# Optimization experiments

Hardware: AMD Instinct MI355X
Metric: run time of the kernel (lower is better)

## Reference

```python
import jax, jax.numpy as jnp
import numpy as np
import math

D_MODEL, NHEAD, D_FF = 1024, 16, 4096
S_TGT, S_MEM, BATCH = 2048, 2048, 2
D_K = D_MODEL // NHEAD
EPS = 1e-5


def _linear_params(key, d_in, d_out):
    kw, kb = jax.random.split(key)
    w = jax.random.normal(kw, (d_in, d_out), jnp.float32) * 0.02
    b = jax.random.normal(kb, (d_out,), jnp.float32) * 0.02
    return w, b


def setup_inputs() -> dict:
    key = jax.random.key(0)
    ks = jax.random.split(key, 16)
    inp = {
        "tgt": jax.random.normal(ks[0], (S_TGT, BATCH, D_MODEL), jnp.float32),
        "memory": jax.random.normal(ks[1], (S_MEM, BATCH, D_MODEL), jnp.float32),
    }
    # self-attn params
    inp["sa_wq"], inp["sa_bq"] = _linear_params(ks[2], D_MODEL, D_MODEL)
    inp["sa_wk"], inp["sa_bk"] = _linear_params(ks[3], D_MODEL, D_MODEL)
    inp["sa_wv"], inp["sa_bv"] = _linear_params(ks[4], D_MODEL, D_MODEL)
    inp["sa_wo"], inp["sa_bo"] = _linear_params(ks[5], D_MODEL, D_MODEL)
    # cross-attn params
    inp["ca_wq"], inp["ca_bq"] = _linear_params(ks[6], D_MODEL, D_MODEL)
    inp["ca_wk"], inp["ca_bk"] = _linear_params(ks[7], D_MODEL, D_MODEL)
    inp["ca_wv"], inp["ca_bv"] = _linear_params(ks[8], D_MODEL, D_MODEL)
    inp["ca_wo"], inp["ca_bo"] = _linear_params(ks[9], D_MODEL, D_MODEL)
    # FFN params
    inp["ff_w1"], inp["ff_b1"] = _linear_params(ks[10], D_MODEL, D_FF)
    inp["ff_w2"], inp["ff_b2"] = _linear_params(ks[11], D_FF, D_MODEL)
    # LayerNorm params
    for i, k in zip((1, 2, 3), (ks[12], ks[13], ks[14])):
        inp[f"ln{i}_g"] = jnp.ones((D_MODEL,), jnp.float32)
        inp[f"ln{i}_b"] = jnp.zeros((D_MODEL,), jnp.float32)
    # masks: causal for self-attn, full for cross-attn (1 = keep, 0 = masked)
    inp["tgt_mask"] = jnp.tril(jnp.ones((S_TGT, S_TGT), jnp.int32))
    inp["memory_mask"] = jnp.ones((S_TGT, S_MEM), jnp.int32)
    return inp


def layer_norm(x, g, b):
    mu = jnp.mean(x, axis=-1, keepdims=True)
    var = jnp.mean(jnp.square(x - mu), axis=-1, keepdims=True)
    return (x - mu) * jax.lax.rsqrt(var + EPS) * g + b


def mha(xq, xkv, wq, bq, wk, bk, wv, bv, wo, bo, mask):
    # xq: [Sq,B,D], xkv: [Sk,B,D], mask: [Sq,Sk] (1 keep / 0 masked)
    Sq, B, _ = xq.shape
    Sk = xkv.shape[0]
    q = (xq @ wq + bq).reshape(Sq, B, NHEAD, D_K)
    k = (xkv @ wk + bk).reshape(Sk, B, NHEAD, D_K)
    v = (xkv @ wv + bv).reshape(Sk, B, NHEAD, D_K)
    scores = jnp.einsum("qbhd,kbhd->bhqk", q, k) / math.sqrt(D_K)
    scores = jnp.where(mask[None, None, :, :] == 0, -1e9, scores)
    attn = jax.nn.softmax(scores, axis=-1)
    ctx = jnp.einsum("bhqk,kbhd->bqhd", attn, v).reshape(B, Sq, D_MODEL)
    out = ctx @ wo + bo  # [B,Sq,D]
    return out.transpose(1, 0, 2)  # [Sq,B,D]


def reference(tgt, memory,
              sa_wq, sa_bq, sa_wk, sa_bk, sa_wv, sa_bv, sa_wo, sa_bo,
              ca_wq, ca_bq, ca_wk, ca_bk, ca_wv, ca_bv, ca_wo, ca_bo,
              ff_w1, ff_b1, ff_w2, ff_b2,
              ln1_g, ln1_b, ln2_g, ln2_b, ln3_g, ln3_b,
              tgt_mask, memory_mask):
    # dropout is identity (eval mode)
    x = tgt + mha(tgt, tgt, sa_wq, sa_bq, sa_wk, sa_bk, sa_wv, sa_bv,
                  sa_wo, sa_bo, tgt_mask)
    x = layer_norm(x, ln1_g, ln1_b)
    x = x + mha(x, memory, ca_wq, ca_bq, ca_wk, ca_bk, ca_wv, ca_bv,
                ca_wo, ca_bo, memory_mask)
    x = layer_norm(x, ln2_g, ln2_b)
    ffn = jax.nn.relu(x @ ff_w1 + ff_b1) @ ff_w2 + ff_b2
    x = layer_norm(x + ffn, ln3_g, ln3_b)
    return x
```

## Files before the change

### kernel.cpp

```cpp
#include <hip/hip_runtime.h>
#include <cstdint>
#include <cstddef>


typedef __bf16 bf16;
typedef __attribute__((ext_vector_type(4))) float f32x4;
typedef __attribute__((ext_vector_type(8))) __bf16 bf16x8;
typedef __attribute__((ext_vector_type(4))) __bf16 bf16x4;
typedef __attribute__((ext_vector_type(2))) __bf16 bf16x2;

#define MFMA(a, b, c) __builtin_amdgcn_mfma_f32_16x16x32_bf16((a), (b), (c), 0, 0, 0)

constexpr int D_MODEL = 1024;
constexpr int S_LEN   = 2048;
constexpr int BATCH   = 2;
constexpr int M_ROWS  = S_LEN * BATCH;

struct bfp { bf16 h, l; };
__device__ __forceinline__ bfp fsplit(float f) {
  bfp r;
  r.h = (bf16)f;
  r.l = (bf16)(f - (float)r.h);
  return r;
}

typedef const void __attribute__((address_space(1))) gas_void;
typedef void __attribute__((address_space(3))) las_void;
__device__ __forceinline__ void glds16(const void* g, void* l) {
  __builtin_amdgcn_global_load_lds((gas_void*)g, (las_void*)l, 16, 0, 0);
}

__global__ void wcast_t(const float* __restrict__ W, bf16* __restrict__ Th,
                        int K, int N) {
  __shared__ float t[32][33];
  const int kt = blockIdx.x * 32, nt = blockIdx.y * 32;
  const int tx = threadIdx.x, ty = threadIdx.y;
#pragma unroll
  for (int i = 0; i < 4; ++i)
    t[ty * 4 + i][tx] = W[(size_t)(kt + ty * 4 + i) * N + nt + tx];
  __syncthreads();
#pragma unroll
  for (int i = 0; i < 4; ++i) {
    int n = nt + ty * 4 + i;
    Th[(size_t)n * K + kt + tx] = (bf16)t[tx][ty * 4 + i];
  }
}

__global__ void act_split(const float* __restrict__ X, bf16* __restrict__ H,
                          bf16* __restrict__ L) {
  const size_t i = ((size_t)blockIdx.x * 256 + threadIdx.x) * 4;
  float4 v = *reinterpret_cast<const float4*>(&X[i]);
  bf16x4 h, l;
  bfp s0 = fsplit(v.x); h[0] = s0.h; l[0] = s0.l;
  bfp s1 = fsplit(v.y); h[1] = s1.h; l[1] = s1.l;
  bfp s2 = fsplit(v.z); h[2] = s2.h; l[2] = s2.l;
  bfp s3 = fsplit(v.w); h[3] = s3.h; l[3] = s3.l;
  *reinterpret_cast<bf16x4*>(&H[i]) = h;
  *reinterpret_cast<bf16x4*>(&L[i]) = l;
}

__launch_bounds__(256)
__global__ void gemm_split(const bf16* __restrict__ Ah_g, const bf16* __restrict__ Al_g,
                           const bf16* __restrict__ Bh_g,
                           const float* __restrict__ bias,
                           float* Cf, bf16* Ch, bf16* Cl,
                           int N, int K, int ldb, int flags) {
  __shared__ bf16 sAh[4096], sAl[4096], sBh[4096];
  const int tid = threadIdx.x, ln = tid & 63, w = tid >> 6;
  const int g = ln >> 4, lr = ln & 15;
  const int wr = w >> 1, wc = w & 1;
  const int m0 = blockIdx.y * 128, n0 = blockIdx.x * 128;
  const int kz = K / gridDim.z;
  const int kbeg = blockIdx.z * kz, kend = kbeg + kz;

  f32x4 acc[4][4] = {};

  for (int k0 = kbeg; k0 < kend; k0 += 32) {
    __syncthreads();
#pragma unroll
    for (int i = 0; i < 2; ++i) {
      const int r = w * 32 + i * 16 + (ln >> 2);
      const int co = (ln & 3) * 8;
      const int lb = (w * 32 + i * 16) * 32;
      glds16(Ah_g + (size_t)(m0 + r) * K + k0 + co, &sAh[lb]);
      glds16(Al_g + (size_t)(m0 + r) * K + k0 + co, &sAl[lb]);
      glds16(Bh_g + (size_t)(n0 + r) * ldb + k0 + co, &sBh[lb]);
    }
    __syncthreads();

    bf16x8 ah[4], al[4], bh[4];
#pragma unroll
    for (int mi = 0; mi < 4; ++mi) {
      const int r = wr * 64 + mi * 16 + lr;
      ah[mi] = *reinterpret_cast<const bf16x8*>(&sAh[r * 32 + g * 8]);
      al[mi] = *reinterpret_cast<const bf16x8*>(&sAl[r * 32 + g * 8]);
    }
#pragma unroll
    for (int ni = 0; ni < 4; ++ni) {
      const int r = wc * 64 + ni * 16 + lr;
      bh[ni] = *reinterpret_cast<const bf16x8*>(&sBh[r * 32 + g * 8]);
    }
#pragma unroll
    for (int mi = 0; mi < 4; ++mi)
#pragma unroll
      for (int ni = 0; ni < 4; ++ni) {
        acc[mi][ni] = MFMA(ah[mi], bh[ni], acc[mi][ni]);
        acc[mi][ni] = MFMA(al[mi], bh[ni], acc[mi][ni]);
      }
  }

  const size_t MN = (size_t)M_ROWS * N;
#pragma unroll
  for (int mi = 0; mi < 4; ++mi)
#pragma unroll
    for (int ni = 0; ni < 4; ++ni) {
      const int col = n0 + wc * 64 + ni * 16 + lr;
      const float bv = ((flags & 16) && blockIdx.z == 0) ? bias[col] : 0.f;
#pragma unroll
      for (int r = 0; r < 4; ++r) {
        const int row = m0 + wr * 64 + mi * 16 + g * 4 + r;
        float v = acc[mi][ni][r] + bv;
        if (flags & 1) v = fmaxf(v, 0.f);
        const size_t off = (size_t)row * N + col;
        if (flags & 32) {
          Cf[blockIdx.z * MN + off] = v;
        } else if (flags & 2) {
          atomicAdd(&Cf[off], v);
        } else if (flags & 4) {
          Ch[off] = (bf16)v;
        } else if (flags & 8) {
          bfp sp = fsplit(v);
          Ch[off] = sp.h;
          Cl[off] = sp.l;
        } else {
          Cf[off] = v;
        }
      }
    }
}

__launch_bounds__(256)
__global__ void attn_kernel(const bf16* __restrict__ Qg, const bf16* __restrict__ Kg,
                            const bf16* __restrict__ Vg, int qs, int kvs,
                            bf16* __restrict__ Ch, bf16* __restrict__ Cl, int causal) {
  __shared__ bf16 Kl[2][64 * 64];
  __shared__ bf16 Vt[2][64][72];
  __shared__ bf16 Pl[4][32][68];
  const int tid = threadIdx.x, ln = tid & 63, w = tid >> 6;
  const int g = ln >> 4, lr = ln & 15;
  const int qt = blockIdx.x, bh = blockIdx.y;
  const int b = bh >> 4, h = bh & 15;
  const int q0 = qt * 128 + w * 32;

  const int krow8 = ln >> 3, d8 = ln & 7;
  const int dq = tid >> 4, kp = tid & 15;

  bf16x8 aq[2][2];
#pragma unroll
  for (int mf = 0; mf < 2; ++mf)
#pragma unroll
    for (int kk = 0; kk < 2; ++kk)
      aq[mf][kk] = *reinterpret_cast<const bf16x8*>(
          &Qg[((size_t)(q0 + mf * 16 + lr) * BATCH + b) * qs + h * 64 + kk * 32 + g * 8]);

  f32x4 acco[2][4] = {};
  float mrun[2][4], lrun[2][4];
#pragma unroll
  for (int mf = 0; mf < 2; ++mf)
#pragma unroll
    for (int r = 0; r < 4; ++r) { mrun[mf][r] = -1e30f; lrun[mf][r] = 0.f; }

  const int nkv = causal ? (qt * 2 + 2) : (S_LEN / 64);

  bf16x4 vreg[2][2];
  auto stageK = [&](int kv0, bf16* dst) {
#pragma unroll
    for (int i = 0; i < 2; ++i) {
      const int rbase = i * 32 + w * 8;
      const int row = rbase + krow8;
      glds16(Kg + (size_t)((kv0 + row) * BATCH + b) * kvs + h * 64 + ((d8 ^ (row & 7)) << 3),
             dst + rbase * 64);
    }
  };
  auto loadV = [&](int kv0) {
#pragma unroll
    for (int p = 0; p < 2; ++p) {
      const int k0v = p * 32 + kp * 2;
      vreg[p][0] = *reinterpret_cast<const bf16x4*>(
          &Vg[(size_t)((kv0 + k0v) * BATCH + b) * kvs + h * 64 + dq * 4]);
      vreg[p][1] = *reinterpret_cast<const bf16x4*>(
          &Vg[(size_t)((kv0 + k0v + 1) * BATCH + b) * kvs + h * 64 + dq * 4]);
    }
  };
  auto writeV = [&](int buf) {
#pragma unroll
    for (int p = 0; p < 2; ++p) {
      const int k0v = p * 32 + kp * 2;
#pragma unroll
      for (int i = 0; i < 4; ++i) {
        bf16x2 t2;
        t2[0] = vreg[p][0][i];
        t2[1] = vreg[p][1][i];
        *reinterpret_cast<bf16x2*>(&Vt[buf][dq * 4 + i][k0v]) = t2;
      }
    }
  };

  stageK(0, Kl[0]);
  loadV(0);
  writeV(0);
  __syncthreads();

  for (int kv = 0; kv < nkv; ++kv) {
    const int cur = kv & 1;
    const bool pre = (kv + 1 < nkv);
    if (pre) {
      stageK((kv + 1) * 64, Kl[cur ^ 1]);
      loadV((kv + 1) * 64);
    }
    const int kv0 = kv * 64;

    if (!(causal && kv0 > q0 + 31)) {
      const char* kbase = (const char*)Kl[cur];
      f32x4 s[2][4];
      __builtin_amdgcn_s_setprio(1);
#pragma unroll
      for (int mf = 0; mf < 2; ++mf)
#pragma unroll
        for (int c = 0; c < 4; ++c) {
          f32x4 a = {};
#pragma unroll
          for (int kk = 0; kk < 2; ++kk) {
            bf16x8 bk = *reinterpret_cast<const bf16x8*>(
                kbase + (c * 16 + lr) * 128 + ((((kk << 2) + g) ^ (lr & 7)) << 4));
            a = MFMA(aq[mf][kk], bk, a);
          }
          s[mf][c] = a;
        }
      __builtin_amdgcn_s_setprio(0);
#pragma unroll
      for (int mf = 0; mf < 2; ++mf)
#pragma unroll
        for (int c = 0; c < 4; ++c)
#pragma unroll
          for (int r = 0; r < 4; ++r) s[mf][c][r] *= 0.125f;

      if (causal && kv0 + 63 > q0) {
#pragma unroll
        for (int mf = 0; mf < 2; ++mf)
#pragma unroll
          for (int c = 0; c < 4; ++c) {
            const int key = kv0 + c * 16 + lr;
#pragma unroll
            for (int r = 0; r < 4; ++r)
              if (key > q0 + mf * 16 + g * 4 + r) s[mf][c][r] = -1e30f;
          }
      }

#pragma unroll
      for (int mf = 0; mf < 2; ++mf)
#pragma unroll
        for (int r = 0; r < 4; ++r) {
          float mx = fmaxf(fmaxf(s[mf][0][r], s[mf][1][r]), fmaxf(s[mf][2][r], s[mf][3][r]));
#pragma unroll
          for (int off = 8; off >= 1; off >>= 1) mx = fmaxf(mx, __shfl_xor(mx, off));
          const float mnew = fmaxf(mrun[mf][r], mx);
          const float sf = __expf(mrun[mf][r] - mnew);
          float pv[4], ps = 0.f;
#pragma unroll
          for (int c = 0; c < 4; ++c) { pv[c] = __expf(s[mf][c][r] - mnew); ps += pv[c]; }
          lrun[mf][r] = lrun[mf][r] * sf + ps;
          mrun[mf][r] = mnew;
#pragma unroll
          for (int t = 0; t < 4; ++t) acco[mf][t][r] *= sf;
#pragma unroll
          for (int c = 0; c < 4; ++c) Pl[w][mf * 16 + g * 4 + r][c * 16 + lr] = (bf16)pv[c];
        }

      __builtin_amdgcn_s_setprio(1);
#pragma unroll
      for (int mf = 0; mf < 2; ++mf) {
        bf16x8 ap0 = *reinterpret_cast<const bf16x8*>(&Pl[w][mf * 16 + lr][g * 8]);
        bf16x8 ap1 = *reinterpret_cast<const bf16x8*>(&Pl[w][mf * 16 + lr][32 + g * 8]);
#pragma unroll
        for (int t = 0; t < 4; ++t) {
          bf16x8 v0 = *reinterpret_cast<const bf16x8*>(&Vt[cur][t * 16 + lr][g * 8]);
          bf16x8 v1 = *reinterpret_cast<const bf16x8*>(&Vt[cur][t * 16 + lr][32 + g * 8]);
          acco[mf][t] = MFMA(ap0, v0, acco[mf][t]);
          acco[mf][t] = MFMA(ap1, v1, acco[mf][t]);
        }
      }
      __builtin_amdgcn_s_setprio(0);
    }

    if (pre) writeV(cur ^ 1);
    __syncthreads();
  }

#pragma unroll
  for (int mf = 0; mf < 2; ++mf)
#pragma unroll
    for (int r = 0; r < 4; ++r) {
      float l = lrun[mf][r];
#pragma unroll
      for (int off = 8; off >= 1; off >>= 1) l += __shfl_xor(l, off);
      lrun[mf][r] = 1.f / l;
    }
#pragma unroll
  for (int mf = 0; mf < 2; ++mf)
#pragma unroll
    for (int t = 0; t < 4; ++t)
#pragma unroll
      for (int r = 0; r < 4; ++r) {
        const int srow = q0 + mf * 16 + g * 4 + r;
        const size_t off = (size_t)(srow * BATCH + b) * D_MODEL + h * 64 + t * 16 + lr;
        const float v = acco[mf][t][r] * lrun[mf][r];
        bfp sp = fsplit(v);
        Ch[off] = sp.h;
        Cl[off] = sp.l;
      }
}

__launch_bounds__(256)
__global__ void add_ln(const float* __restrict__ X, const float* __restrict__ Y0,
                       const float* __restrict__ Y1,
                       const float* __restrict__ gam, const float* __restrict__ bet,
                       float* __restrict__ O, bf16* __restrict__ Oh, bf16* __restrict__ Ol) {
  const int row = blockIdx.x, tid = threadIdx.x;
  const int lane = tid & 63, w = tid >> 6;
  __shared__ float red[4];
  float4 x = *reinterpret_cast<const float4*>(&X[(size_t)row * D_MODEL + tid * 4]);
  float4 y = *reinterpret_cast<const float4*>(&Y0[(size_t)row * D_MODEL + tid * 4]);
  float v0 = x.x + y.x, v1 = x.y + y.y, v2 = x.z + y.z, v3 = x.w + y.w;
  if (Y1) {
    float4 z = *reinterpret_cast<const float4*>(&Y1[(size_t)row * D_MODEL + tid * 4]);
    v0 += z.x; v1 += z.y; v2 += z.z; v3 += z.w;
  }
  float sm = v0 + v1 + v2 + v3;
#pragma unroll
  for (int off = 32; off >= 1; off >>= 1) sm += __shfl_xor(sm, off);
  if (lane == 0) red[w] = sm;
  __syncthreads();
  float mu = (red[0] + red[1] + red[2] + red[3]) * (1.f / D_MODEL);
  float d0 = v0 - mu, d1 = v1 - mu, d2 = v2 - mu, d3 = v3 - mu;
  float qs = d0 * d0 + d1 * d1 + d2 * d2 + d3 * d3;
#pragma unroll
  for (int off = 32; off >= 1; off >>= 1) qs += __shfl_xor(qs, off);
  __syncthreads();
  if (lane == 0) red[w] = qs;
  __syncthreads();
  float var = (red[0] + red[1] + red[2] + red[3]) * (1.f / D_MODEL);
  float rs = rsqrtf(var + 1e-5f);
  float4 gv = *reinterpret_cast<const float4*>(&gam[tid * 4]);
  float4 bv = *reinterpret_cast<const float4*>(&bet[tid * 4]);
  float4 o;
  o.x = d0 * rs * gv.x + bv.x;
  o.y = d1 * rs * gv.y + bv.y;
  o.z = d2 * rs * gv.z + bv.z;
  o.w = d3 * rs * gv.w + bv.w;
  *reinterpret_cast<float4*>(&O[(size_t)row * D_MODEL + tid * 4]) = o;
  if (Oh) {
    bf16x4 h4, l4;
    bfp s0 = fsplit(o.x); h4[0] = s0.h; l4[0] = s0.l;
    bfp s1 = fsplit(o.y); h4[1] = s1.h; l4[1] = s1.l;
    bfp s2 = fsplit(o.z); h4[2] = s2.h; l4[2] = s2.l;
    bfp s3 = fsplit(o.w); h4[3] = s3.h; l4[3] = s3.l;
    *reinterpret_cast<bf16x4*>(&Oh[(size_t)row * D_MODEL + tid * 4]) = h4;
    *reinterpret_cast<bf16x4*>(&Ol[(size_t)row * D_MODEL + tid * 4]) = l4;
  }
}

extern "C" void kernel_launch(void* const* d_in, const int* in_sizes, int n_in,
                              void* d_out, int out_size, void* d_ws, size_t ws_size,
                              hipStream_t stream) {
  (void)in_sizes; (void)n_in; (void)out_size; (void)ws_size;
  const float* tgt   = (const float*)d_in[0];
  const float* mem   = (const float*)d_in[1];
  const float* sa_wq = (const float*)d_in[2];
  const float* sa_bq = (const float*)d_in[3];
  const float* sa_wk = (const float*)d_in[4];
  const float* sa_bk = (const float*)d_in[5];
  const float* sa_wv = (const float*)d_in[6];
  const float* sa_bv = (const float*)d_in[7];
  const float* sa_wo = (const float*)d_in[8];
  const float* sa_bo = (const float*)d_in[9];
  const float* ca_wq = (const float*)d_in[10];
  const float* ca_bq = (const float*)d_in[11];
  const float* ca_wk = (const float*)d_in[12];
  const float* ca_bk = (const float*)d_in[13];
  const float* ca_wv = (const float*)d_in[14];
  const float* ca_bv = (const float*)d_in[15];
  const float* ca_wo = (const float*)d_in[16];
  const float* ca_bo = (const float*)d_in[17];
  const float* ff_w1 = (const float*)d_in[18];
  const float* ff_b1 = (const float*)d_in[19];
  const float* ff_w2 = (const float*)d_in[20];
  const float* ff_b2 = (const float*)d_in[21];
  const float* ln1g  = (const float*)d_in[22];
  const float* ln1b  = (const float*)d_in[23];
  const float* ln2g  = (const float*)d_in[24];
  const float* ln2b  = (const float*)d_in[25];
  const float* ln3g  = (const float*)d_in[26];
  const float* ln3b  = (const float*)d_in[27];
  float* out = (float*)d_out;

  char* base = (char*)d_ws;
  const size_t MB = 1u << 20;
  auto B16 = [&](size_t mb) { return (bf16*)(base + mb * MB); };
  auto F32 = [&](size_t mb) { return (float*)(base + mb * MB); };

  bf16 *qkvW_h  = B16(0);
  bf16 *sawo_h  = B16(6);
  bf16 *caqW_h  = B16(8);
  bf16 *cakvW_h = B16(10);
  bf16 *cawo_h  = B16(14);
  bf16 *w1_h    = B16(16);
  bf16 *w2_h    = B16(24);
  float* qkv_bias  = F32(32);
  float* cakv_bias = (float*)(base + 32 * MB + 65536);
  bf16 *tgt_h = B16(33), *tgt_l = B16(41);
  bf16 *mem_h = B16(49), *mem_l = B16(57);
  bf16 *QKV   = B16(65);
  bf16 *Qb    = B16(65);
  bf16 *KVb   = B16(73);
  bf16 *HC_h  = B16(65), *HC_l = B16(81);
  bf16 *CTX_h = B16(89), *CTX_l = B16(97);
  float* X1f  = F32(105);
  float* ACC  = F32(121);
  float* ACC2 = F32(137);
  float* X2f  = F32(153);

  dim3 cb(32, 8);
  auto cast_w = [&](const float* W, int K, int N, bf16* th) {
    hipLaunchKernelGGL(wcast_t, dim3(K / 32, N / 32), cb, 0, stream, W, th, K, N);
  };
  cast_w(sa_wq, 1024, 1024, qkvW_h);
  cast_w(sa_wk, 1024, 1024, qkvW_h + (size_t)1024 * 1024);
  cast_w(sa_wv, 1024, 1024, qkvW_h + (size_t)2048 * 1024);
  cast_w(sa_wo, 1024, 1024, sawo_h);
  cast_w(ca_wq, 1024, 1024, caqW_h);
  cast_w(ca_wk, 1024, 1024, cakvW_h);
  cast_w(ca_wv, 1024, 1024, cakvW_h + (size_t)1024 * 1024);
  cast_w(ca_wo, 1024, 1024, cawo_h);
  cast_w(ff_w1, 1024, 4096, w1_h);
  cast_w(ff_w2, 4096, 1024, w2_h);
  hipMemcpyAsync(qkv_bias,        sa_bq, 4096, hipMemcpyDeviceToDevice, stream);
  hipMemcpyAsync(qkv_bias + 1024, sa_bk, 4096, hipMemcpyDeviceToDevice, stream);
  hipMemcpyAsync(qkv_bias + 2048, sa_bv, 4096, hipMemcpyDeviceToDevice, stream);
  hipMemcpyAsync(cakv_bias,        ca_bk, 4096, hipMemcpyDeviceToDevice, stream);
  hipMemcpyAsync(cakv_bias + 1024, ca_bv, 4096, hipMemcpyDeviceToDevice, stream);
  hipLaunchKernelGGL(act_split, dim3(4096), dim3(256), 0, stream, tgt, tgt_h, tgt_l);
  hipLaunchKernelGGL(act_split, dim3(4096), dim3(256), 0, stream, mem, mem_h, mem_l);

  auto gemm = [&](const bf16* ah, const bf16* al, const bf16* bh,
                  const float* bias, float* cf, bf16* ch, bf16* cl,
                  int N, int K, int ldb, int flags, int Z) {
    hipLaunchKernelGGL(gemm_split, dim3(N / 128, 32, Z), dim3(256), 0, stream,
                       ah, al, bh, bias, cf, ch, cl, N, K, ldb, flags);
  };
  const size_t FBYTES = (size_t)M_ROWS * D_MODEL * 4;

  gemm(tgt_h, tgt_l, qkvW_h, qkv_bias, nullptr, QKV, nullptr, 3072, 1024, 1024, 4 | 16, 1);
  hipLaunchKernelGGL(attn_kernel, dim3(S_LEN / 128, 32), dim3(256), 0, stream,
                     QKV, QKV + 1024, QKV + 2048, 3072, 3072, CTX_h, CTX_l, 1);
  gemm(CTX_h, CTX_l, sawo_h, sa_bo, ACC, nullptr, nullptr, 1024, 1024, 1024, 32 | 16, 2);
  hipLaunchKernelGGL(add_ln, dim3(M_ROWS), dim3(256), 0, stream,
                     tgt, ACC, ACC2, ln1g, ln1b, X1f, CTX_h, CTX_l);

  gemm(CTX_h, CTX_l, caqW_h, ca_bq, nullptr, Qb, nullptr, 1024, 1024, 1024, 4 | 16, 1);
  gemm(mem_h, mem_l, cakvW_h, cakv_bias, nullptr, KVb, nullptr, 2048, 1024, 1024, 4 | 16, 1);
  hipLaunchKernelGGL(attn_kernel, dim3(S_LEN / 128, 32), dim3(256), 0, stream,
                     Qb, KVb, KVb + 1024, 1024, 2048, CTX_h, CTX_l, 0);
  gemm(CTX_h, CTX_l, cawo_h, ca_bo, ACC, nullptr, nullptr, 1024, 1024, 1024, 32 | 16, 2);
  hipLaunchKernelGGL(add_ln, dim3(M_ROWS), dim3(256), 0, stream,
                     X1f, ACC, ACC2, ln2g, ln2b, X2f, tgt_h, tgt_l);

  hipMemsetAsync(ACC, 0, FBYTES, stream);
  for (int c = 0; c < 2; ++c) {
    gemm(tgt_h, tgt_l, w1_h + (size_t)c * 2048 * 1024, ff_b1 + c * 2048,
         nullptr, HC_h, HC_l, 2048, 1024, 1024, 8 | 16 | 1, 1);
    gemm(HC_h, HC_l, w2_h + c * 2048, ff_b2, ACC, nullptr, nullptr,
         1024, 2048, 4096, 2 | (c == 0 ? 16 : 0), 2);
  }
  hipLaunchKernelGGL(add_ln, dim3(M_ROWS), dim3(256), 0, stream,
                     X2f, ACC, nullptr, ln3g, ln3b, out, nullptr, nullptr);
}
```

Before: 937.7 us.

## Fold softmax scale into K weights, lazy rescale, atomic split-K GEMMs, unchunked FFN

```diff
diff --git a/kernel.cpp b/kernel.cpp
--- a/kernel.cpp
+++ b/kernel.cpp
@@ -31,7 +31,7 @@
 }
 
 __global__ void wcast_t(const float* __restrict__ W, bf16* __restrict__ Th,
-                        int K, int N) {
+                        int K, int N, float sc) {
   __shared__ float t[32][33];
   const int kt = blockIdx.x * 32, nt = blockIdx.y * 32;
   const int tx = threadIdx.x, ty = threadIdx.y;
@@ -42,8 +42,14 @@
 #pragma unroll
   for (int i = 0; i < 4; ++i) {
     int n = nt + ty * 4 + i;
-    Th[(size_t)n * K + kt + tx] = (bf16)t[tx][ty * 4 + i];
+    Th[(size_t)n * K + kt + tx] = (bf16)(t[tx][ty * 4 + i] * sc);
   }
+}
+
+__global__ void scale_copy(const float* __restrict__ S, float* __restrict__ D,
+                           float sc) {
+  const int i = blockIdx.x * 256 + threadIdx.x;
+  D[i] = S[i] * sc;
 }
 
 __global__ void act_split(const float* __restrict__ X, bf16* __restrict__ H,
@@ -57,6 +63,14 @@
   bfp s3 = fsplit(v.w); h[3] = s3.h; l[3] = s3.l;
   *reinterpret_cast<bf16x4*>(&H[i]) = h;
   *reinterpret_cast<bf16x4*>(&L[i]) = l;
+}
+
+__global__ void cast_bf16(const float* __restrict__ X, bf16* __restrict__ H) {
+  const size_t i = ((size_t)blockIdx.x * 256 + threadIdx.x) * 4;
+  float4 v = *reinterpret_cast<const float4*>(&X[i]);
+  bf16x4 h;
+  h[0] = (bf16)v.x; h[1] = (bf16)v.y; h[2] = (bf16)v.z; h[3] = (bf16)v.w;
+  *reinterpret_cast<bf16x4*>(&H[i]) = h;
 }
 
 __launch_bounds__(256)
@@ -109,7 +123,6 @@
       }
   }
 
-  const size_t MN = (size_t)M_ROWS * N;
 #pragma unroll
   for (int mi = 0; mi < 4; ++mi)
 #pragma unroll
@@ -122,9 +135,7 @@
         float v = acc[mi][ni][r] + bv;
         if (flags & 1) v = fmaxf(v, 0.f);
         const size_t off = (size_t)row * N + col;
-        if (flags & 32) {
-          Cf[blockIdx.z * MN + off] = v;
-        } else if (flags & 2) {
+        if (flags & 2) {
           atomicAdd(&Cf[off], v);
         } else if (flags & 4) {
           Ch[off] = (bf16)v;
@@ -238,12 +249,6 @@
           s[mf][c] = a;
         }
       __builtin_amdgcn_s_setprio(0);
-#pragma unroll
-      for (int mf = 0; mf < 2; ++mf)
-#pragma unroll
-        for (int c = 0; c < 4; ++c)
-#pragma unroll
-          for (int r = 0; r < 4; ++r) s[mf][c][r] *= 0.125f;
 
       if (causal && kv0 + 63 > q0) {
 #pragma unroll
@@ -257,22 +262,40 @@
           }
       }
 
+      float lm[2][4];
+      bool need = false;
 #pragma unroll
       for (int mf = 0; mf < 2; ++mf)
 #pragma unroll
         for (int r = 0; r < 4; ++r) {
-          float mx = fmaxf(fmaxf(s[mf][0][r], s[mf][1][r]), fmaxf(s[mf][2][r], s[mf][3][r]));
-#pragma unroll
-          for (int off = 8; off >= 1; off >>= 1) mx = fmaxf(mx, __shfl_xor(mx, off));
-          const float mnew = fmaxf(mrun[mf][r], mx);
-          const float sf = __expf(mrun[mf][r] - mnew);
+          lm[mf][r] = fmaxf(fmaxf(s[mf][0][r], s[mf][1][r]),
+                            fmaxf(s[mf][2][r], s[mf][3][r]));
+          need = need || (lm[mf][r] > mrun[mf][r] + 5.f);
+        }
+      if (__any(need)) {
+#pragma unroll
+        for (int mf = 0; mf < 2; ++mf)
+#pragma unroll
+          for (int r = 0; r < 4; ++r) {
+            float mx = lm[mf][r];
+#pragma unroll
+            for (int off = 8; off >= 1; off >>= 1) mx = fmaxf(mx, __shfl_xor(mx, off));
+            const float mnew = fmaxf(mrun[mf][r], mx);
+            const float sf = __expf(mrun[mf][r] - mnew);
+            lrun[mf][r] *= sf;
+            mrun[mf][r] = mnew;
+#pragma unroll
+            for (int t = 0; t < 4; ++t) acco[mf][t][r] *= sf;
+          }
+      }
+#pragma unroll
+      for (int mf = 0; mf < 2; ++mf)
+#pragma unroll
+        for (int r = 0; r < 4; ++r) {
           float pv[4], ps = 0.f;
 #pragma unroll
-          for (int c = 0; c < 4; ++c) { pv[c] = __expf(s[mf][c][r] - mnew); ps += pv[c]; }
-          lrun[mf][r] = lrun[mf][r] * sf + ps;
-          mrun[mf][r] = mnew;
-#pragma unroll
-          for (int t = 0; t < 4; ++t) acco[mf][t][r] *= sf;
+          for (int c = 0; c < 4; ++c) { pv[c] = __expf(s[mf][c][r] - mrun[mf][r]); ps += pv[c]; }
+          lrun[mf][r] += ps;
 #pragma unroll
           for (int c = 0; c < 4; ++c) Pl[w][mf * 16 + g * 4 + r][c * 16 + lr] = (bf16)pv[c];
         }
@@ -423,32 +446,31 @@
   bf16 *QKV   = B16(65);
   bf16 *Qb    = B16(65);
   bf16 *KVb   = B16(73);
-  bf16 *HC_h  = B16(65), *HC_l = B16(81);
+  bf16 *HC_h  = B16(49), *HC_l = B16(81);
   bf16 *CTX_h = B16(89), *CTX_l = B16(97);
   float* X1f  = F32(105);
-  float* ACC  = F32(121);
-  float* ACC2 = F32(137);
-  float* X2f  = F32(153);
+  float* X2f  = F32(121);
+  float* ACC  = F32(137);
 
   dim3 cb(32, 8);
-  auto cast_w = [&](const float* W, int K, int N, bf16* th) {
-    hipLaunchKernelGGL(wcast_t, dim3(K / 32, N / 32), cb, 0, stream, W, th, K, N);
+  auto cast_w = [&](const float* W, int K, int N, bf16* th, float sc) {
+    hipLaunchKernelGGL(wcast_t, dim3(K / 32, N / 32), cb, 0, stream, W, th, K, N, sc);
   };
-  cast_w(sa_wq, 1024, 1024, qkvW_h);
-  cast_w(sa_wk, 1024, 1024, qkvW_h + (size_t)1024 * 1024);
-  cast_w(sa_wv, 1024, 1024, qkvW_h + (size_t)2048 * 1024);
-  cast_w(sa_wo, 1024, 1024, sawo_h);
-  cast_w(ca_wq, 1024, 1024, caqW_h);
-  cast_w(ca_wk, 1024, 1024, cakvW_h);
-  cast_w(ca_wv, 1024, 1024, cakvW_h + (size_t)1024 * 1024);
-  cast_w(ca_wo, 1024, 1024, cawo_h);
-  cast_w(ff_w1, 1024, 4096, w1_h);
-  cast_w(ff_w2, 4096, 1024, w2_h);
-  hipMemcpyAsync(qkv_bias,        sa_bq, 4096, hipMemcpyDeviceToDevice, stream);
-  hipMemcpyAsync(qkv_bias + 1024, sa_bk, 4096, hipMemcpyDeviceToDevice, stream);
-  hipMemcpyAsync(qkv_bias + 2048, sa_bv, 4096, hipMemcpyDeviceToDevice, stream);
-  hipMemcpyAsync(cakv_bias,        ca_bk, 4096, hipMemcpyDeviceToDevice, stream);
-  hipMemcpyAsync(cakv_bias + 1024, ca_bv, 4096, hipMemcpyDeviceToDevice, stream);
+  cast_w(sa_wq, 1024, 1024, qkvW_h, 1.f);
+  cast_w(sa_wk, 1024, 1024, qkvW_h + (size_t)1024 * 1024, 0.125f);
+  cast_w(sa_wv, 1024, 1024, qkvW_h + (size_t)2048 * 1024, 1.f);
+  cast_w(sa_wo, 1024, 1024, sawo_h, 1.f);
+  cast_w(ca_wq, 1024, 1024, caqW_h, 1.f);
+  cast_w(ca_wk, 1024, 1024, cakvW_h, 0.125f);
+  cast_w(ca_wv, 1024, 1024, cakvW_h + (size_t)1024 * 1024, 1.f);
+  cast_w(ca_wo, 1024, 1024, cawo_h, 1.f);
+  cast_w(ff_w1, 1024, 4096, w1_h, 1.f);
+  cast_w(ff_w2, 4096, 1024, w2_h, 1.f);
+  hipLaunchKernelGGL(scale_copy, dim3(4), dim3(256), 0, stream, sa_bq, qkv_bias, 1.f);
+  hipLaunchKernelGGL(scale_copy, dim3(4), dim3(256), 0, stream, sa_bk, qkv_bias + 1024, 0.125f);
+  hipLaunchKernelGGL(scale_copy, dim3(4), dim3(256), 0, stream, sa_bv, qkv_bias + 2048, 1.f);
+  hipLaunchKernelGGL(scale_copy, dim3(4), dim3(256), 0, stream, ca_bk, cakv_bias, 0.125f);
+  hipLaunchKernelGGL(scale_copy, dim3(4), dim3(256), 0, stream, ca_bv, cakv_bias + 1024, 1.f);
   hipLaunchKernelGGL(act_split, dim3(4096), dim3(256), 0, stream, tgt, tgt_h, tgt_l);
   hipLaunchKernelGGL(act_split, dim3(4096), dim3(256), 0, stream, mem, mem_h, mem_l);
 
@@ -463,25 +485,25 @@
   gemm(tgt_h, tgt_l, qkvW_h, qkv_bias, nullptr, QKV, nullptr, 3072, 1024, 1024, 4 | 16, 1);
   hipLaunchKernelGGL(attn_kernel, dim3(S_LEN / 128, 32), dim3(256), 0, stream,
                      QKV, QKV + 1024, QKV + 2048, 3072, 3072, CTX_h, CTX_l, 1);
-  gemm(CTX_h, CTX_l, sawo_h, sa_bo, ACC, nullptr, nullptr, 1024, 1024, 1024, 32 | 16, 2);
+  hipMemsetAsync(ACC, 0, FBYTES, stream);
+  gemm(CTX_h, CTX_l, sawo_h, sa_bo, ACC, nullptr, nullptr, 1024, 1024, 1024, 2 | 16, 4);
   hipLaunchKernelGGL(add_ln, dim3(M_ROWS), dim3(256), 0, stream,
-                     tgt, ACC, ACC2, ln1g, ln1b, X1f, CTX_h, CTX_l);
-
-  gemm(CTX_h, CTX_l, caqW_h, ca_bq, nullptr, Qb, nullptr, 1024, 1024, 1024, 4 | 16, 1);
+                     tgt, ACC, nullptr, ln1g, ln1b, X1f, CTX_h, CTX_l);
+
+  hipMemsetAsync(ACC, 0, FBYTES, stream);
+  gemm(CTX_h, CTX_l, caqW_h, ca_bq, ACC, nullptr, nullptr, 1024, 1024, 1024, 2 | 16, 4);
+  hipLaunchKernelGGL(cast_bf16, dim3(4096), dim3(256), 0, stream, ACC, Qb);
   gemm(mem_h, mem_l, cakvW_h, cakv_bias, nullptr, KVb, nullptr, 2048, 1024, 1024, 4 | 16, 1);
   hipLaunchKernelGGL(attn_kernel, dim3(S_LEN / 128, 32), dim3(256), 0, stream,
                      Qb, KVb, KVb + 1024, 1024, 2048, CTX_h, CTX_l, 0);
-  gemm(CTX_h, CTX_l, cawo_h, ca_bo, ACC, nullptr, nullptr, 1024, 1024, 1024, 32 | 16, 2);
+  hipMemsetAsync(ACC, 0, FBYTES, stream);
+  gemm(CTX_h, CTX_l, cawo_h, ca_bo, ACC, nullptr, nullptr, 1024, 1024, 1024, 2 | 16, 4);
   hipLaunchKernelGGL(add_ln, dim3(M_ROWS), dim3(256), 0, stream,
-                     X1f, ACC, ACC2, ln2g, ln2b, X2f, tgt_h, tgt_l);
-
+                     X1f, ACC, nullptr, ln2g, ln2b, X2f, tgt_h, tgt_l);
+
+  gemm(tgt_h, tgt_l, w1_h, ff_b1, nullptr, HC_h, HC_l, 4096, 1024, 1024, 8 | 16 | 1, 1);
   hipMemsetAsync(ACC, 0, FBYTES, stream);
-  for (int c = 0; c < 2; ++c) {
-    gemm(tgt_h, tgt_l, w1_h + (size_t)c * 2048 * 1024, ff_b1 + c * 2048,
-         nullptr, HC_h, HC_l, 2048, 1024, 1024, 8 | 16 | 1, 1);
-    gemm(HC_h, HC_l, w2_h + c * 2048, ff_b2, ACC, nullptr, nullptr,
-         1024, 2048, 4096, 2 | (c == 0 ? 16 : 0), 2);
-  }
+  gemm(HC_h, HC_l, w2_h, ff_b2, ACC, nullptr, nullptr, 1024, 4096, 4096, 2 | 16, 4);
   hipLaunchKernelGGL(add_ln, dim3(M_ROWS), dim3(256), 0, stream,
                      X2f, ACC, nullptr, ln3g, ln3b, out, nullptr, nullptr);
 }
```

Result: slower. 1.019 ms (+8.6%).
